# Kernel tuning notes

Hardware: AMD Instinct MI355X
Metric: run time of the kernel (lower is better)

The kernel has to match this reference:

```python
import jax, jax.numpy as jnp
import numpy as np

B, C, H, W = 4, 384, 248, 216
NUM_ANCHORS = 6           # len(rotations)=2 * len(sizes)=3
NUM_CLASSES = 3
BOX_CODE_SIZE = 7
CLS_OUT = NUM_ANCHORS * NUM_CLASSES      # 18
REG_OUT = NUM_ANCHORS * BOX_CODE_SIZE    # 42
DIR_OUT = NUM_ANCHORS * 2                # 12


def setup_inputs() -> dict:
    key = jax.random.key(0)
    ks = jax.random.split(key, 4)
    x = jax.random.normal(ks[0], (B, C, H, W), dtype=jnp.float32)
    scale = 0.02
    w_cls = jax.random.normal(ks[1], (C, CLS_OUT), dtype=jnp.float32) * scale
    w_reg = jax.random.normal(ks[2], (C, REG_OUT), dtype=jnp.float32) * scale
    w_dir = jax.random.normal(ks[3], (C, DIR_OUT), dtype=jnp.float32) * scale
    b_cls = jnp.zeros((CLS_OUT,), dtype=jnp.float32)
    b_reg = jnp.zeros((REG_OUT,), dtype=jnp.float32)
    b_dir = jnp.zeros((DIR_OUT,), dtype=jnp.float32)
    return {"x": x, "w_cls": w_cls, "b_cls": b_cls, "w_reg": w_reg,
            "b_reg": b_reg, "w_dir": w_dir, "b_dir": b_dir}


def _conv1x1(x, w, b):
    # channels_first 1x1 conv == per-pixel matmul over channels
    return jnp.einsum('bchw,co->bohw', x, w) + b[None, :, None, None]


def reference(x, w_cls, b_cls, w_reg, b_reg, w_dir, b_dir):
    cls_score = _conv1x1(x, w_cls, b_cls)      # [B, 18, H, W]
    bbox_pred = _conv1x1(x, w_reg, b_reg)      # [B, 42, H, W]
    dir_cls_preds = _conv1x1(x, w_dir, b_dir)  # [B, 12, H, W]
    return (cls_score, bbox_pred, dir_cls_preds)
```

## Files before the change

### kernel.cpp

```cpp
#include <hip/hip_runtime.h>


constexpr int Bn   = 4;
constexpr int Cc   = 384;
constexpr int Hh   = 248;
constexpr int Ww   = 216;
constexpr int HW   = Hh * Ww;
constexpr int NPIX = Bn * HW;
constexpr int NCLS = 18;
constexpr int NREG = 42;
constexpr int NDIR = 12;

template<int NA, int LDA, int NB, int LDB>
__device__ __forceinline__ void cohort_run(
    const float* __restrict__ xb,
    const float* __restrict__ wA, const float* __restrict__ bA,
    float* __restrict__ oA,
    const float* __restrict__ wB, const float* __restrict__ bB,
    float* __restrict__ oB)
{
    float acc[NA + NB];
    #pragma unroll
    for (int j = 0; j < NA; ++j) acc[j] = bA[j];
    #pragma unroll
    for (int j = 0; j < NB; ++j) acc[NA + j] = bB[j];

    #pragma unroll 4
    for (int c = 0; c < Cc; ++c) {
        const float xv = xb[(size_t)c * HW];
        #pragma unroll
        for (int j = 0; j < NA; ++j)
            acc[j] = fmaf(xv, wA[c * LDA + j], acc[j]);
        #pragma unroll
        for (int j = 0; j < NB; ++j)
            acc[NA + j] = fmaf(xv, wB[c * LDB + j], acc[NA + j]);
    }

    #pragma unroll
    for (int j = 0; j < NA; ++j) oA[(size_t)j * HW] = acc[j];
    #pragma unroll
    for (int j = 0; j < NB; ++j) oB[(size_t)j * HW] = acc[NA + j];
}

__global__ __launch_bounds__(256) void head_fused_msplit(
    const float* __restrict__ x,
    const float* __restrict__ wc, const float* __restrict__ bc,
    const float* __restrict__ wr, const float* __restrict__ br,
    const float* __restrict__ wd, const float* __restrict__ bd,
    float* __restrict__ out)
{
    const int w    = threadIdx.x >> 6;
    const int lane = threadIdx.x & 63;
    const int pix  = blockIdx.x * 64 + lane;
    const int b    = pix / HW;
    const int p    = pix - b * HW;

    const float* __restrict__ xb = x + (size_t)b * Cc * HW + p;

    float* __restrict__ outc = out + (size_t)b * NCLS * HW + p;
    float* __restrict__ outr = out + (size_t)Bn * NCLS * HW
                                   + (size_t)b * NREG * HW + p;
    float* __restrict__ outd = out + (size_t)Bn * (NCLS + NREG) * HW
                                   + (size_t)b * NDIR * HW + p;

    if (w == 0) {
        cohort_run<18, NCLS, 0, 1>(xb, wc, bc, outc, wc, bc, outc);
    } else if (w == 1) {
        cohort_run<18, NREG, 0, 1>(xb, wr, br, outr, wr, br, outr);
    } else if (w == 2) {
        cohort_run<18, NREG, 0, 1>(xb, wr + 18, br + 18, outr + (size_t)18 * HW,
                                   wr, br, outr);
    } else {
        cohort_run<6, NREG, 12, NDIR>(xb, wr + 36, br + 36, outr + (size_t)36 * HW,
                                      wd, bd, outd);
    }
}

extern "C" void kernel_launch(void* const* d_in, const int* in_sizes, int n_in,
                              void* d_out, int out_size, void* d_ws, size_t ws_size,
                              hipStream_t stream) {
    const float* x  = (const float*)d_in[0];
    const float* wc = (const float*)d_in[1];
    const float* bc = (const float*)d_in[2];
    const float* wr = (const float*)d_in[3];
    const float* br = (const float*)d_in[4];
    const float* wd = (const float*)d_in[5];
    const float* bd = (const float*)d_in[6];
    float* out = (float*)d_out;

    dim3 grid(NPIX / 64);
    dim3 block(256);
    head_fused_msplit<<<grid, block, 0, stream>>>(x, wc, bc, wr, br, wd, bd, out);
}
```

Measured before the change: 531.5 us.

## Compute fused 1x1-conv head with bf16 MFMA and pre-packed transposed weights

Adds a prep kernel that transposes, concatenates and pads the three weight matrices to 80 outputs in bf16, along with a padded bias vector. A new main kernel converts each pixel's channel values to bf16, stages them in LDS, and runs 16x16x32 bf16 MFMAs, so each wave covers 64 pixels by 80 outputs. This replaces the scalar fp32 FMA path, where four waves each re-read the same x column. It lowers precision to bf16 inputs with fp32 accumulation, and falls back to the old kernel if the workspace is too small.

```diff
diff --git a/kernel.cpp b/kernel.cpp
--- a/kernel.cpp
+++ b/kernel.cpp
@@ -10,32 +10,136 @@
 constexpr int NCLS = 18;
 constexpr int NREG = 42;
 constexpr int NDIR = 12;
+constexpr int NPAD = 80;
+constexpr int CP   = 40;
+
+typedef __attribute__((ext_vector_type(8))) short short8;
+typedef __attribute__((ext_vector_type(4))) float f32x4;
+
+__device__ __forceinline__ unsigned short f2bf(float f) {
+    unsigned u = __float_as_uint(f);
+    u += 0x7FFFu + ((u >> 16) & 1u);
+    return (unsigned short)(u >> 16);
+}
+
+__global__ __launch_bounds__(256) void head_prep(
+    const float* __restrict__ wc, const float* __restrict__ bc,
+    const float* __restrict__ wr, const float* __restrict__ br,
+    const float* __restrict__ wd, const float* __restrict__ bd,
+    unsigned short* __restrict__ Wt, float* __restrict__ biasp)
+{
+    int e = blockIdx.x * 256 + threadIdx.x;
+    int o = e / Cc, c = e - o * Cc;
+    float v = 0.f;
+    if (o < NCLS)            v = wc[c * NCLS + o];
+    else if (o < NCLS+NREG)  v = wr[c * NREG + (o - NCLS)];
+    else if (o < 72)         v = wd[c * NDIR + (o - NCLS - NREG)];
+    Wt[e] = f2bf(v);
+    if (e < NPAD) {
+        float bv = 0.f;
+        if (e < NCLS)           bv = bc[e];
+        else if (e < NCLS+NREG) bv = br[e - NCLS];
+        else if (e < 72)        bv = bd[e - NCLS - NREG];
+        biasp[e] = bv;
+    }
+}
+
+__global__ __launch_bounds__(256) void head_mfma(
+    const float* __restrict__ x,
+    const unsigned short* __restrict__ Wt,
+    const float* __restrict__ biasp,
+    float* __restrict__ out)
+{
+    __shared__ short lds[256 * CP];
+
+    const int w    = threadIdx.x >> 6;
+    const int lane = threadIdx.x & 63;
+    const int n    = lane & 15;
+    const int q    = lane >> 4;
+
+    const int wpx0 = blockIdx.x * 256 + w * 64;
+    const int mypx = wpx0 + lane;
+    const int sb   = mypx / HW;
+    const int sp   = mypx - sb * HW;
+    const float* __restrict__ xs = x + (size_t)sb * (Cc * HW) + sp;
+
+    short* __restrict__ myrow = &lds[(w * 64 + lane) * CP];
+
+    float bias_t[5];
+    #pragma unroll
+    for (int t = 0; t < 5; ++t) bias_t[t] = biasp[16 * t + n];
+
+    f32x4 acc[4][5] = {};
+
+    #pragma unroll 2
+    for (int k0 = 0; k0 < Cc; k0 += 32) {
+        #pragma unroll
+        for (int g = 0; g < 4; ++g) {
+            float xv[8];
+            #pragma unroll
+            for (int i = 0; i < 8; ++i)
+                xv[i] = xs[(size_t)(k0 + g * 8 + i) * HW];
+            short8 pk;
+            #pragma unroll
+            for (int i = 0; i < 8; ++i) pk[i] = (short)f2bf(xv[i]);
+            *(short8*)(myrow + g * 8) = pk;
+        }
+        short8 bf[5];
+        #pragma unroll
+        for (int t = 0; t < 5; ++t)
+            bf[t] = *(const short8*)(Wt + (size_t)(16 * t + n) * Cc + k0 + q * 8);
+        #pragma unroll
+        for (int st = 0; st < 4; ++st) {
+            short8 af = *(const short8*)(&lds[(w * 64 + st * 16 + n) * CP + q * 8]);
+            #pragma unroll
+            for (int t = 0; t < 5; ++t)
+                acc[st][t] = __builtin_amdgcn_mfma_f32_16x16x32_bf16(
+                                 af, bf[t], acc[st][t], 0, 0, 0);
+        }
+    }
+
+    #pragma unroll
+    for (int st = 0; st < 4; ++st) {
+        const int px = wpx0 + st * 16;
+        const int bb = px / HW;
+        const int pp = px - bb * HW;
+        #pragma unroll
+        for (int t = 0; t < 5; ++t) {
+            const int o = 16 * t + n;
+            float* rowp;
+            if (o < NCLS)
+                rowp = out + ((size_t)bb * NCLS + o) * HW;
+            else if (o < NCLS + NREG)
+                rowp = out + (size_t)Bn * NCLS * HW + ((size_t)bb * NREG + (o - NCLS)) * HW;
+            else
+                rowp = out + (size_t)Bn * (NCLS + NREG) * HW + ((size_t)bb * NDIR + (o - 60)) * HW;
+            f32x4 v = acc[st][t];
+            v[0] += bias_t[t]; v[1] += bias_t[t]; v[2] += bias_t[t]; v[3] += bias_t[t];
+            if (o < 72)
+                *(f32x4*)(rowp + pp + q * 4) = v;
+        }
+    }
+}
 
 template<int NA, int LDA, int NB, int LDB>
 __device__ __forceinline__ void cohort_run(
     const float* __restrict__ xb,
-    const float* __restrict__ wA, const float* __restrict__ bA,
-    float* __restrict__ oA,
-    const float* __restrict__ wB, const float* __restrict__ bB,
-    float* __restrict__ oB)
+    const float* __restrict__ wA, const float* __restrict__ bA, float* __restrict__ oA,
+    const float* __restrict__ wB, const float* __restrict__ bB, float* __restrict__ oB)
 {
     float acc[NA + NB];
     #pragma unroll
     for (int j = 0; j < NA; ++j) acc[j] = bA[j];
     #pragma unroll
     for (int j = 0; j < NB; ++j) acc[NA + j] = bB[j];
-
     #pragma unroll 4
     for (int c = 0; c < Cc; ++c) {
         const float xv = xb[(size_t)c * HW];
         #pragma unroll
-        for (int j = 0; j < NA; ++j)
-            acc[j] = fmaf(xv, wA[c * LDA + j], acc[j]);
+        for (int j = 0; j < NA; ++j) acc[j] = fmaf(xv, wA[c * LDA + j], acc[j]);
         #pragma unroll
-        for (int j = 0; j < NB; ++j)
-            acc[NA + j] = fmaf(xv, wB[c * LDB + j], acc[NA + j]);
+        for (int j = 0; j < NB; ++j) acc[NA + j] = fmaf(xv, wB[c * LDB + j], acc[NA + j]);
     }
-
     #pragma unroll
     for (int j = 0; j < NA; ++j) oA[(size_t)j * HW] = acc[j];
     #pragma unroll
@@ -49,31 +153,17 @@
     const float* __restrict__ wd, const float* __restrict__ bd,
     float* __restrict__ out)
 {
-    const int w    = threadIdx.x >> 6;
-    const int lane = threadIdx.x & 63;
-    const int pix  = blockIdx.x * 64 + lane;
-    const int b    = pix / HW;
-    const int p    = pix - b * HW;
-
+    const int w = threadIdx.x >> 6, lane = threadIdx.x & 63;
+    const int pix = blockIdx.x * 64 + lane;
+    const int b = pix / HW, p = pix - b * HW;
     const float* __restrict__ xb = x + (size_t)b * Cc * HW + p;
-
     float* __restrict__ outc = out + (size_t)b * NCLS * HW + p;
-    float* __restrict__ outr = out + (size_t)Bn * NCLS * HW
-                                   + (size_t)b * NREG * HW + p;
-    float* __restrict__ outd = out + (size_t)Bn * (NCLS + NREG) * HW
-                                   + (size_t)b * NDIR * HW + p;
-
-    if (w == 0) {
-        cohort_run<18, NCLS, 0, 1>(xb, wc, bc, outc, wc, bc, outc);
-    } else if (w == 1) {
-        cohort_run<18, NREG, 0, 1>(xb, wr, br, outr, wr, br, outr);
-    } else if (w == 2) {
-        cohort_run<18, NREG, 0, 1>(xb, wr + 18, br + 18, outr + (size_t)18 * HW,
-                                   wr, br, outr);
-    } else {
-        cohort_run<6, NREG, 12, NDIR>(xb, wr + 36, br + 36, outr + (size_t)36 * HW,
-                                      wd, bd, outd);
-    }
+    float* __restrict__ outr = out + (size_t)Bn * NCLS * HW + (size_t)b * NREG * HW + p;
+    float* __restrict__ outd = out + (size_t)Bn * (NCLS + NREG) * HW + (size_t)b * NDIR * HW + p;
+    if (w == 0)      cohort_run<18, NCLS, 0, 1>(xb, wc, bc, outc, wc, bc, outc);
+    else if (w == 1) cohort_run<18, NREG, 0, 1>(xb, wr, br, outr, wr, br, outr);
+    else if (w == 2) cohort_run<18, NREG, 0, 1>(xb, wr + 18, br + 18, outr + (size_t)18 * HW, wr, br, outr);
+    else             cohort_run<6, NREG, 12, NDIR>(xb, wr + 36, br + 36, outr + (size_t)36 * HW, wd, bd, outd);
 }
 
 extern "C" void kernel_launch(void* const* d_in, const int* in_sizes, int n_in,
@@ -88,7 +178,18 @@
     const float* bd = (const float*)d_in[6];
     float* out = (float*)d_out;
 
-    dim3 grid(NPIX / 64);
-    dim3 block(256);
-    head_fused_msplit<<<grid, block, 0, stream>>>(x, wc, bc, wr, br, wd, bd, out);
+    const size_t wt_bytes   = (size_t)NPAD * Cc * sizeof(unsigned short);
+    const size_t bias_off   = wt_bytes;
+    const size_t need_bytes = bias_off + NPAD * sizeof(float);
+
+    if (ws_size >= need_bytes) {
+        unsigned short* Wt = (unsigned short*)d_ws;
+        float* biasp = (float*)((char*)d_ws + bias_off);
+        head_prep<<<dim3((NPAD * Cc) / 256), dim3(256), 0, stream>>>(
+            wc, bc, wr, br, wd, bd, Wt, biasp);
+        head_mfma<<<dim3(NPIX / 256), dim3(256), 0, stream>>>(x, Wt, biasp, out);
+    } else {
+        head_fused_msplit<<<dim3(NPIX / 64), dim3(256), 0, stream>>>(
+            x, wc, bc, wr, br, wd, bd, out);
+    }
 }
```

New measurement: 571.2 us. 7.5% more time.
